# Performance work log

Hardware: AMD Instinct MI355X
Metric: run time of the kernel (lower is better)

The kernel has to match this reference:

```python
import jax, jax.numpy as jnp
import numpy as np

H = 4096
NUM_HEADS = 32
D = 128
SEQ_LEN = 1024
CTX = 4096


def setup_inputs() -> dict:
    key = jax.random.key(0)
    k1, k2, k3, k4 = jax.random.split(key, 4)
    X = jax.random.normal(k1, (SEQ_LEN, H), dtype=jnp.float32)
    # Linear weight [out=3H, in=H]; scale ~1/sqrt(H) so attention logits are O(1)
    W = jax.random.normal(k2, (3 * H, H), dtype=jnp.float32) * (1.0 / np.sqrt(H))
    cache_K = jax.random.normal(k3, (1, CTX, NUM_HEADS, D), dtype=jnp.float32)
    cache_V = jax.random.normal(k4, (1, CTX, NUM_HEADS, D), dtype=jnp.float32)
    return {"X": X, "W": W, "cache_K": cache_K, "cache_V": cache_V}


def reference(X, W, cache_K, cache_V):
    seq_len, h = X.shape
    nh, d = cache_K.shape[2], cache_K.shape[3]
    # fused QKV projection (Linear, no bias): X @ W^T -> [seq_len, 3H]
    qkv = X @ W.T
    q, k, v = jnp.split(qkv, 3, axis=1)
    q = q.reshape(1, seq_len, nh, d)
    k = k.reshape(1, seq_len, nh, d)
    v = v.reshape(1, seq_len, nh, d)
    # concat KV cache along the sequence dim (cache_K[:, :P] with P = full cache)
    k_full = jnp.concatenate([cache_K, k], axis=1)  # [1, ctx+seq, nh, d]
    v_full = jnp.concatenate([cache_V, v], axis=1)
    scale = 1.0 / np.sqrt(d)
    # scores: [1, nh, seq_q, kv_len]
    scores = jnp.einsum("bqhd,bkhd->bhqk", q, k_full) * scale
    weights = jax.nn.softmax(scores, axis=-1)
    out = jnp.einsum("bhqk,bkhd->bqhd", weights, v_full)  # [1, seq, nh, d]
    return out.reshape(seq_len, h)
```

## Files before the change

### kernel.cpp

```cpp
#include <hip/hip_runtime.h>
#include <hip/hip_bf16.h>
#include <stdint.h>

#define H_DIM 4096
#define NH 32
#define HD 128
#define SEQ 1024
#define CTX 4096
#define KVL (CTX + SEQ)
#define W3H (3 * H_DIM)
#define ATTN_SCALE 0.08838834764831845f

typedef short short8 __attribute__((ext_vector_type(8)));
typedef float f32x4 __attribute__((ext_vector_type(4)));

#define GLOAD_LDS16(g, l)                                             \
  __builtin_amdgcn_global_load_lds(                                   \
      (const __attribute__((address_space(1))) void*)(g),             \
      (__attribute__((address_space(3))) void*)(l), 16, 0, 0)

__device__ __forceinline__ unsigned short f2b(float f) {
  union { float f; unsigned u; } v; v.f = f;
  return (unsigned short)((v.u + 0x7FFFu + ((v.u >> 16) & 1u)) >> 16);
}
__device__ __forceinline__ float b2f(unsigned short u) {
  union { unsigned u; float f; } v; v.u = ((unsigned)u) << 16;
  return v.f;
}

__global__ void k_cvt(const float* __restrict__ s, unsigned short* __restrict__ d, int n4) {
  int i = blockIdx.x * blockDim.x + threadIdx.x;
  if (i >= n4) return;
  float4 v = reinterpret_cast<const float4*>(s)[i];
  ushort4 o;
  o.x = f2b(v.x); o.y = f2b(v.y); o.z = f2b(v.z); o.w = f2b(v.w);
  reinterpret_cast<ushort4*>(d)[i] = o;
}

#define BM 128
#define BN 128
#define BK 64
__global__ __launch_bounds__(256, 2) void k_gemm_qkv(
    const unsigned short* __restrict__ A,
    const unsigned short* __restrict__ B,
    unsigned short* __restrict__ C) {
  __shared__ unsigned short As[BM * BK];
  __shared__ unsigned short Bs[BN * BK];
  const int tid = threadIdx.x;
  const int lane = tid & 63;
  const int wid = tid >> 6;
  const int bn = blockIdx.x, bm = blockIdx.y;
  const int wr = wid >> 1, wc = wid & 1;

  f32x4 acc[4][4] = {};

  const int lrow = lane >> 3;
  const int lcol = (lane & 7) * 8;
  const unsigned short* ga = A + (size_t)(bm * BM + wid * 32 + lrow) * H_DIM + lcol;
  const unsigned short* gb = B + (size_t)(bn * BN + wid * 32 + lrow) * H_DIM + lcol;

  for (int kt = 0; kt < H_DIM / BK; ++kt) {
    __syncthreads();
    const unsigned short* gak = ga + kt * BK;
    const unsigned short* gbk = gb + kt * BK;
#pragma unroll
    for (int i = 0; i < 4; ++i) {
      GLOAD_LDS16(gak + i * 8 * H_DIM, As + (wid * 4 + i) * 512);
      GLOAD_LDS16(gbk + i * 8 * H_DIM, Bs + (wid * 4 + i) * 512);
    }
    __syncthreads();
#pragma unroll
    for (int kk = 0; kk < 2; ++kk) {
      short8 af[4], bfr[4];
#pragma unroll
      for (int m = 0; m < 4; ++m)
        af[m] = *reinterpret_cast<const short8*>(
            As + (wr * 64 + m * 16 + (lane & 15)) * BK + kk * 32 + (lane >> 4) * 8);
#pragma unroll
      for (int n = 0; n < 4; ++n)
        bfr[n] = *reinterpret_cast<const short8*>(
            Bs + (wc * 64 + n * 16 + (lane & 15)) * BK + kk * 32 + (lane >> 4) * 8);
#pragma unroll
      for (int m = 0; m < 4; ++m)
#pragma unroll
        for (int n = 0; n < 4; ++n)
          acc[m][n] = __builtin_amdgcn_mfma_f32_16x16x32_bf16(af[m], bfr[n], acc[m][n], 0, 0, 0);
    }
  }
  const int r0 = bm * BM + wr * 64 + (lane >> 4) * 4;
  const int c0 = bn * BN + wc * 64 + (lane & 15);
#pragma unroll
  for (int m = 0; m < 4; ++m)
#pragma unroll
    for (int n = 0; n < 4; ++n)
#pragma unroll
      for (int r = 0; r < 4; ++r)
        C[(size_t)(r0 + m * 16 + r) * W3H + c0 + n * 16] = f2b(acc[m][n][r]);
}

__global__ void k_build_k(const float* __restrict__ cK, const unsigned short* __restrict__ QKV,
                          unsigned short* __restrict__ Kb) {
  int idx = (blockIdx.x * 256 + threadIdx.x) * 4;
  if (idx >= NH * KVL * HD) return;
  int h = idx / (KVL * HD);
  int rem = idx % (KVL * HD);
  int kv = rem / HD;
  int d = rem % HD;
  ushort4 o;
  if (kv < CTX) {
    float4 v = *reinterpret_cast<const float4*>(cK + ((size_t)kv * NH + h) * HD + d);
    o.x = f2b(v.x); o.y = f2b(v.y); o.z = f2b(v.z); o.w = f2b(v.w);
  } else {
    o = *reinterpret_cast<const ushort4*>(QKV + (size_t)(kv - CTX) * W3H + H_DIM + h * HD + d);
  }
  *reinterpret_cast<ushort4*>(Kb + idx) = o;
}

__global__ void k_build_vt(const float* __restrict__ cV, const unsigned short* __restrict__ QKV,
                           unsigned short* __restrict__ Vt) {
  __shared__ unsigned short T[HD][66];
  const int h = blockIdx.y;
  const int kt = blockIdx.x;
  const int t = threadIdx.x;
#pragma unroll
  for (int e = 0; e < 8; ++e) {
    int idx = (t + e * 256) * 4;
    int kvl = idx >> 7;
    int d = idx & 127;
    int kv = kt * 64 + kvl;
    unsigned short a, b, c, w;
    if (kv < CTX) {
      float4 v = *reinterpret_cast<const float4*>(cV + ((size_t)kv * NH + h) * HD + d);
      a = f2b(v.x); b = f2b(v.y); c = f2b(v.z); w = f2b(v.w);
    } else {
      ushort4 u = *reinterpret_cast<const ushort4*>(QKV + (size_t)(kv - CTX) * W3H + 2 * H_DIM + h * HD + d);
      a = u.x; b = u.y; c = u.z; w = u.w;
    }
    T[d][kvl] = a; T[d + 1][kvl] = b; T[d + 2][kvl] = c; T[d + 3][kvl] = w;
  }
  __syncthreads();
#pragma unroll
  for (int e = 0; e < 8; ++e) {
    int idx = (t + e * 256) * 4;
    int d = idx >> 6;
    int kv0 = idx & 63;
    ushort4 o;
    o.x = T[d][kv0]; o.y = T[d][kv0 + 1]; o.z = T[d][kv0 + 2]; o.w = T[d][kv0 + 3];
    *reinterpret_cast<ushort4*>(Vt + ((size_t)h * HD + d) * KVL + kt * 64 + kv0) = o;
  }
}

#define KVT 64
#define NT (KVL / KVT)
#define NT2 (NT / 2)
__global__ __launch_bounds__(256, 2) void k_attn(
    const unsigned short* __restrict__ QKV,
    const unsigned short* __restrict__ Kb,
    const unsigned short* __restrict__ Vt,
    float* __restrict__ A0,
    float* __restrict__ A1,
    float* __restrict__ Mp,
    float* __restrict__ Lp) {
  __shared__ unsigned short Ks[2][KVT * HD];
  __shared__ unsigned short Vs[2][KVT * HD];
  const int tid = threadIdx.x, lane = tid & 63, wid = tid >> 6;
  const int g = lane >> 4;
  const int qi = lane & 15;
  const int id = blockIdx.x;
  const int xcd = id & 7, slot = id >> 3;
  const int h = xcd * 4 + (slot >> 4);
  const int rem = slot & 15;
  const int qt = rem >> 1;
  const int split = rem & 1;
  const int kt0 = split * NT2;
  const int q0 = qt * 128 + wid * 32;

  short8 qf[2][4];
#pragma unroll
  for (int hf = 0; hf < 2; ++hf)
#pragma unroll
    for (int c = 0; c < 4; ++c) {
      short8 q = *reinterpret_cast<const short8*>(
          QKV + (size_t)(q0 + hf * 16 + qi) * W3H + h * HD + c * 32 + g * 8);
      short8 t;
#pragma unroll
      for (int j = 0; j < 8; ++j) t[j] = (short)f2b(b2f((unsigned short)q[j]) * ATTN_SCALE);
      qf[hf][c] = t;
    }

  float m_r[2] = {-1e30f, -1e30f}, l_r[2] = {0.f, 0.f};
  f32x4 acc_o[2][8] = {};

  const char* Kh = (const char*)(Kb + (size_t)h * KVL * HD);
  const char* Vh = (const char*)(Vt + (size_t)h * HD * KVL);

  short8 rK[4], rV[4];

#define LOADR(t)                                                               \
  {                                                                            \
    _Pragma("unroll") for (int i = 0; i < 4; ++i) {                            \
      int c = wid * 4 + i;                                                     \
      int krow = c * 4 + (lane >> 4);                                          \
      int klcb = (16 * (lane & 15)) ^ ((krow & 7) << 4);                       \
      rK[i] = *reinterpret_cast<const short8*>(                                \
          Kh + (size_t)((t) * KVT + krow) * 256 + klcb);                       \
      int vrow = c * 8 + (lane >> 3);                                          \
      int vlcb = (16 * (lane & 7)) ^ ((vrow & 7) << 4);                        \
      rV[i] = *reinterpret_cast<const short8*>(                                \
          Vh + (size_t)vrow * (KVL * 2) + (size_t)(t) * 128 + vlcb);           \
    }                                                                          \
  }
#define WRITE_LDS(b)                                                           \
  {                                                                            \
    _Pragma("unroll") for (int i = 0; i < 4; ++i) {                            \
      *reinterpret_cast<short8*>((char*)Ks[b] + (wid * 4 + i) * 1024 + lane * 16) = rK[i]; \
      *reinterpret_cast<short8*>((char*)Vs[b] + (wid * 4 + i) * 1024 + lane * 16) = rV[i]; \
    }                                                                          \
  }

  LOADR(kt0);
  WRITE_LDS(0);
  __syncthreads();

  const int i0 = ((2 * (g & 1) + 0) * 16 + qi) * 4;
  const int i1 = ((2 * (g & 1) + 1) * 16 + qi) * 4;

  for (int kt = 0; kt < NT2; ++kt) {
    const int cur = kt & 1;
    if (kt + 1 < NT2) LOADR(kt0 + kt + 1);

    f32x4 s[2][4] = {};
#pragma unroll
    for (int n = 0; n < 4; ++n) {
      int row = n * 16 + qi;
#pragma unroll
      for (int c = 0; c < 4; ++c) {
        int cb = (c * 32 + g * 8) * 2;
        short8 kf = *reinterpret_cast<const short8*>(
            (const char*)Ks[cur] + row * 256 + (cb ^ ((row & 7) << 4)));
        s[0][n] = __builtin_amdgcn_mfma_f32_16x16x32_bf16(kf, qf[0][c], s[0][n], 0, 0, 0);
        s[1][n] = __builtin_amdgcn_mfma_f32_16x16x32_bf16(kf, qf[1][c], s[1][n], 0, 0, 0);
      }
    }

    float p[2][4][4];
    int ok = 1;
    float tmax[2];
#pragma unroll
    for (int hf = 0; hf < 2; ++hf) {
      float t0 = s[hf][0][0];
#pragma unroll
      for (int n = 0; n < 4; ++n)
#pragma unroll
        for (int r = 0; r < 4; ++r) t0 = fmaxf(t0, s[hf][n][r]);
      t0 = fmaxf(t0, __shfl_xor(t0, 16, 64));
      t0 = fmaxf(t0, __shfl_xor(t0, 32, 64));
      tmax[hf] = t0;
      ok &= (t0 <= m_r[hf] + 8.0f);
    }
    if (!__all(ok)) {
#pragma unroll
      for (int hf = 0; hf < 2; ++hf) {
        float mn = fmaxf(m_r[hf], tmax[hf]);
        float alpha = __expf(m_r[hf] - mn);
        l_r[hf] *= alpha;
        m_r[hf] = mn;
#pragma unroll
        for (int nd = 0; nd < 8; ++nd) acc_o[hf][nd] *= alpha;
      }
    }
#pragma unroll
    for (int hf = 0; hf < 2; ++hf) {
      float sum = 0.f;
#pragma unroll
      for (int n = 0; n < 4; ++n)
#pragma unroll
        for (int r = 0; r < 4; ++r) {
          p[hf][n][r] = __expf(s[hf][n][r] - m_r[hf]);
          sum += p[hf][n][r];
        }
      sum += __shfl_xor(sum, 16, 64);
      sum += __shfl_xor(sum, 32, 64);
      l_r[hf] += sum;
    }

    unsigned pr[2][4][2];
#pragma unroll
    for (int hf = 0; hf < 2; ++hf)
#pragma unroll
      for (int n = 0; n < 4; ++n)
#pragma unroll
        for (int rr = 0; rr < 2; ++rr) {
          union { __hip_bfloat162 b; unsigned u; } cv;
          cv.b = __float22bfloat162_rn(make_float2(p[hf][n][2 * rr], p[hf][n][2 * rr + 1]));
          pr[hf][n][rr] = cv.u;
        }

#pragma unroll
    for (int kc = 0; kc < 2; ++kc) {
      short8 pv[2];
#pragma unroll
      for (int hf = 0; hf < 2; ++hf) {
        int a0 = __builtin_amdgcn_ds_bpermute(i0, (int)pr[hf][2 * kc][0]);
        int b0 = __builtin_amdgcn_ds_bpermute(i0, (int)pr[hf][2 * kc + 1][0]);
        int a1 = __builtin_amdgcn_ds_bpermute(i0, (int)pr[hf][2 * kc][1]);
        int b1 = __builtin_amdgcn_ds_bpermute(i0, (int)pr[hf][2 * kc + 1][1]);
        int a2 = __builtin_amdgcn_ds_bpermute(i1, (int)pr[hf][2 * kc][0]);
        int b2 = __builtin_amdgcn_ds_bpermute(i1, (int)pr[hf][2 * kc + 1][0]);
        int a3 = __builtin_amdgcn_ds_bpermute(i1, (int)pr[hf][2 * kc][1]);
        int b3 = __builtin_amdgcn_ds_bpermute(i1, (int)pr[hf][2 * kc + 1][1]);
        union { int i[4]; short8 s8; } u;
        u.i[0] = (g < 2) ? a0 : b0;
        u.i[1] = (g < 2) ? a1 : b1;
        u.i[2] = (g < 2) ? a2 : b2;
        u.i[3] = (g < 2) ? a3 : b3;
        pv[hf] = u.s8;
      }

#pragma unroll
      for (int nd = 0; nd < 8; ++nd) {
        int row = nd * 16 + qi;
        int cb = kc * 64 + g * 16;
        short8 vf = *reinterpret_cast<const short8*>(
            (const char*)Vs[cur] + row * 128 + (cb ^ ((row & 7) << 4)));
        acc_o[0][nd] = __builtin_amdgcn_mfma_f32_16x16x32_bf16(vf, pv[0], acc_o[0][nd], 0, 0, 0);
        acc_o[1][nd] = __builtin_amdgcn_mfma_f32_16x16x32_bf16(vf, pv[1], acc_o[1][nd], 0, 0, 0);
      }
    }

    if (kt + 1 < NT2) WRITE_LDS(cur ^ 1);
    __syncthreads();
  }

  float* Op = split ? A1 : A0;
#pragma unroll
  for (int hf = 0; hf < 2; ++hf) {
    float* orow = Op + (size_t)(q0 + hf * 16 + qi) * H_DIM + h * HD;
#pragma unroll
    for (int nd = 0; nd < 8; ++nd)
      *reinterpret_cast<float4*>(orow + nd * 16 + g * 4) =
          *reinterpret_cast<const float4*>(&acc_o[hf][nd]);
    if (g == 0) {
      int q = q0 + hf * 16 + qi;
      Mp[split * (NH * SEQ) + h * SEQ + q] = m_r[hf];
      Lp[split * (NH * SEQ) + h * SEQ + q] = l_r[hf];
    }
  }
#undef LOADR
#undef WRITE_LDS
}

__global__ void k_combine(const float* __restrict__ A1, const float* __restrict__ Mp,
                          const float* __restrict__ Lp, float* __restrict__ out) {
  int i4 = blockIdx.x * 256 + threadIdx.x;
  int q = i4 >> 10;
  int c4 = i4 & 1023;
  int h = c4 >> 5;
  float m0 = Mp[h * SEQ + q], m1 = Mp[NH * SEQ + h * SEQ + q];
  float l0 = Lp[h * SEQ + q], l1 = Lp[NH * SEQ + h * SEQ + q];
  float M = fmaxf(m0, m1);
  float w0 = __expf(m0 - M), w1 = __expf(m1 - M);
  float inv = 1.0f / (w0 * l0 + w1 * l1);
  float4 a0 = reinterpret_cast<const float4*>(out)[i4];
  float4 a1 = reinterpret_cast<const float4*>(A1)[i4];
  float4 o;
  o.x = (w0 * a0.x + w1 * a1.x) * inv;
  o.y = (w0 * a0.y + w1 * a1.y) * inv;
  o.z = (w0 * a0.z + w1 * a1.z) * inv;
  o.w = (w0 * a0.w + w1 * a1.w) * inv;
  reinterpret_cast<float4*>(out)[i4] = o;
}

extern "C" void kernel_launch(void* const* d_in, const int* in_sizes, int n_in,
                              void* d_out, int out_size, void* d_ws, size_t ws_size,
                              hipStream_t stream) {
  const float* X = (const float*)d_in[0];
  const float* W = (const float*)d_in[1];
  const float* cK = (const float*)d_in[2];
  const float* cV = (const float*)d_in[3];
  float* out = (float*)d_out;
  char* ws = (char*)d_ws;

  unsigned short* Xb = (unsigned short*)(ws);
  float* Mp = (float*)(ws);
  float* Lp = (float*)(ws + (256 << 10));
  unsigned short* QKVb = (unsigned short*)(ws + ((size_t)8 << 20));
  unsigned short* Wb = (unsigned short*)(ws + ((size_t)32 << 20));
  unsigned short* Kb = (unsigned short*)(ws + ((size_t)32 << 20));
  unsigned short* Vt = (unsigned short*)(ws + ((size_t)72 << 20));
  float* A1 = (float*)(ws + ((size_t)112 << 20));

  k_cvt<<<(SEQ * H_DIM / 4) / 256, 256, 0, stream>>>(X, Xb, SEQ * H_DIM / 4);
  k_cvt<<<(W3H * H_DIM / 4) / 256, 256, 0, stream>>>(W, Wb, W3H * H_DIM / 4);

  dim3 gg(W3H / BN, SEQ / BM);
  k_gemm_qkv<<<gg, 256, 0, stream>>>(Xb, Wb, QKVb);

  k_build_k<<<(NH * KVL * HD / 4) / 256, 256, 0, stream>>>(cK, QKVb, Kb);
  dim3 gv(KVL / 64, NH);
  k_build_vt<<<gv, 256, 0, stream>>>(cV, QKVb, Vt);

  k_attn<<<SEQ / 128 * NH * 2, 256, 0, stream>>>(QKVb, Kb, Vt, out, A1, Mp, Lp);
  k_combine<<<(SEQ * H_DIM / 4) / 256, 256, 0, stream>>>(A1, Mp, Lp, out);
}
```

Baseline: 351.1 us.

## Software-pipeline attention with async global-to-LDS loads and merge conversion kernels

The attention loop now stages K and V tiles with direct global-to-LDS loads instead of going through registers. Loads are issued two tiles ahead, and the QK^T MFMAs for the next tile are interleaved with the softmax and PV work of the current tile. MFMA sections are wrapped in s_setprio so that matrix work gets issue priority. The two fp32-to-bf16 conversion launches are also merged into one kernel to cut launch overhead. In exchange, register pressure rises from the two live score buffers, and correctness depends on the barriers being placed right relative to the async LDS writes.

```diff
diff --git a/kernel.cpp b/kernel.cpp
--- a/kernel.cpp
+++ b/kernel.cpp
@@ -28,13 +28,20 @@
   return v.f;
 }
 
-__global__ void k_cvt(const float* __restrict__ s, unsigned short* __restrict__ d, int n4) {
-  int i = blockIdx.x * blockDim.x + threadIdx.x;
-  if (i >= n4) return;
-  float4 v = reinterpret_cast<const float4*>(s)[i];
+__global__ void k_cvt2(const float* __restrict__ X, const float* __restrict__ W,
+                       unsigned short* __restrict__ Xb, unsigned short* __restrict__ Wb) {
+  const int nx = SEQ * H_DIM / 4;
+  const int nw = W3H * H_DIM / 4;
+  int i = blockIdx.x * 256 + threadIdx.x;
+  const float* s;
+  unsigned short* d;
+  int j;
+  if (i < nx) { s = X; d = Xb; j = i; }
+  else { j = i - nx; if (j >= nw) return; s = W; d = Wb; }
+  float4 v = reinterpret_cast<const float4*>(s)[j];
   ushort4 o;
   o.x = f2b(v.x); o.y = f2b(v.y); o.z = f2b(v.z); o.w = f2b(v.w);
-  reinterpret_cast<ushort4*>(d)[i] = o;
+  reinterpret_cast<ushort4*>(d)[j] = o;
 }
 
 #define BM 128
@@ -194,142 +201,146 @@
   const char* Kh = (const char*)(Kb + (size_t)h * KVL * HD);
   const char* Vh = (const char*)(Vt + (size_t)h * HD * KVL);
 
-  short8 rK[4], rV[4];
-
-#define LOADR(t)                                                               \
+#define STAGE_K(t, b)                                                          \
   {                                                                            \
     _Pragma("unroll") for (int i = 0; i < 4; ++i) {                            \
       int c = wid * 4 + i;                                                     \
       int krow = c * 4 + (lane >> 4);                                          \
       int klcb = (16 * (lane & 15)) ^ ((krow & 7) << 4);                       \
-      rK[i] = *reinterpret_cast<const short8*>(                                \
-          Kh + (size_t)((t) * KVT + krow) * 256 + klcb);                       \
+      GLOAD_LDS16(Kh + (size_t)((t) * KVT + krow) * 256 + klcb,                \
+                  (char*)Ks[b] + c * 1024);                                    \
+    }                                                                          \
+  }
+#define STAGE_V(t, b)                                                          \
+  {                                                                            \
+    _Pragma("unroll") for (int i = 0; i < 4; ++i) {                            \
+      int c = wid * 4 + i;                                                     \
       int vrow = c * 8 + (lane >> 3);                                          \
       int vlcb = (16 * (lane & 7)) ^ ((vrow & 7) << 4);                        \
-      rV[i] = *reinterpret_cast<const short8*>(                                \
-          Vh + (size_t)vrow * (KVL * 2) + (size_t)(t) * 128 + vlcb);           \
-    }                                                                          \
-  }
-#define WRITE_LDS(b)                                                           \
+      GLOAD_LDS16(Vh + (size_t)vrow * (KVL * 2) + (size_t)(t) * 128 + vlcb,    \
+                  (char*)Vs[b] + c * 1024);                                    \
+    }                                                                          \
+  }
+#define QKT(buf, S)                                                            \
   {                                                                            \
-    _Pragma("unroll") for (int i = 0; i < 4; ++i) {                            \
-      *reinterpret_cast<short8*>((char*)Ks[b] + (wid * 4 + i) * 1024 + lane * 16) = rK[i]; \
-      *reinterpret_cast<short8*>((char*)Vs[b] + (wid * 4 + i) * 1024 + lane * 16) = rV[i]; \
-    }                                                                          \
-  }
-
-  LOADR(kt0);
-  WRITE_LDS(0);
-  __syncthreads();
+    _Pragma("unroll") for (int n = 0; n < 4; ++n) {                            \
+      S[0][n] = (f32x4){0.f, 0.f, 0.f, 0.f};                                   \
+      S[1][n] = (f32x4){0.f, 0.f, 0.f, 0.f};                                   \
+    }                                                                          \
+    __builtin_amdgcn_s_setprio(1);                                             \
+    _Pragma("unroll") for (int n = 0; n < 4; ++n) {                            \
+      int row = n * 16 + qi;                                                   \
+      _Pragma("unroll") for (int c = 0; c < 4; ++c) {                          \
+        int cb = (c * 32 + g * 8) * 2;                                         \
+        short8 kf = *reinterpret_cast<const short8*>(                          \
+            (const char*)Ks[buf] + row * 256 + (cb ^ ((row & 7) << 4)));       \
+        S[0][n] = __builtin_amdgcn_mfma_f32_16x16x32_bf16(kf, qf[0][c], S[0][n], 0, 0, 0); \
+        S[1][n] = __builtin_amdgcn_mfma_f32_16x16x32_bf16(kf, qf[1][c], S[1][n], 0, 0, 0); \
+      }                                                                        \
+    }                                                                          \
+    __builtin_amdgcn_s_setprio(0);                                             \
+  }
 
   const int i0 = ((2 * (g & 1) + 0) * 16 + qi) * 4;
   const int i1 = ((2 * (g & 1) + 1) * 16 + qi) * 4;
 
-  for (int kt = 0; kt < NT2; ++kt) {
-    const int cur = kt & 1;
-    if (kt + 1 < NT2) LOADR(kt0 + kt + 1);
-
-    f32x4 s[2][4] = {};
-#pragma unroll
-    for (int n = 0; n < 4; ++n) {
-      int row = n * 16 + qi;
-#pragma unroll
-      for (int c = 0; c < 4; ++c) {
-        int cb = (c * 32 + g * 8) * 2;
-        short8 kf = *reinterpret_cast<const short8*>(
-            (const char*)Ks[cur] + row * 256 + (cb ^ ((row & 7) << 4)));
-        s[0][n] = __builtin_amdgcn_mfma_f32_16x16x32_bf16(kf, qf[0][c], s[0][n], 0, 0, 0);
-        s[1][n] = __builtin_amdgcn_mfma_f32_16x16x32_bf16(kf, qf[1][c], s[1][n], 0, 0, 0);
-      }
-    }
-
-    float p[2][4][4];
-    int ok = 1;
-    float tmax[2];
-#pragma unroll
-    for (int hf = 0; hf < 2; ++hf) {
-      float t0 = s[hf][0][0];
-#pragma unroll
-      for (int n = 0; n < 4; ++n)
-#pragma unroll
-        for (int r = 0; r < 4; ++r) t0 = fmaxf(t0, s[hf][n][r]);
-      t0 = fmaxf(t0, __shfl_xor(t0, 16, 64));
-      t0 = fmaxf(t0, __shfl_xor(t0, 32, 64));
-      tmax[hf] = t0;
-      ok &= (t0 <= m_r[hf] + 8.0f);
-    }
-    if (!__all(ok)) {
-#pragma unroll
-      for (int hf = 0; hf < 2; ++hf) {
-        float mn = fmaxf(m_r[hf], tmax[hf]);
-        float alpha = __expf(m_r[hf] - mn);
-        l_r[hf] *= alpha;
-        m_r[hf] = mn;
-#pragma unroll
-        for (int nd = 0; nd < 8; ++nd) acc_o[hf][nd] *= alpha;
-      }
-    }
-#pragma unroll
-    for (int hf = 0; hf < 2; ++hf) {
-      float sum = 0.f;
-#pragma unroll
-      for (int n = 0; n < 4; ++n)
-#pragma unroll
-        for (int r = 0; r < 4; ++r) {
-          p[hf][n][r] = __expf(s[hf][n][r] - m_r[hf]);
-          sum += p[hf][n][r];
-        }
-      sum += __shfl_xor(sum, 16, 64);
-      sum += __shfl_xor(sum, 32, 64);
-      l_r[hf] += sum;
-    }
-
-    unsigned pr[2][4][2];
-#pragma unroll
-    for (int hf = 0; hf < 2; ++hf)
-#pragma unroll
-      for (int n = 0; n < 4; ++n)
-#pragma unroll
-        for (int rr = 0; rr < 2; ++rr) {
-          union { __hip_bfloat162 b; unsigned u; } cv;
-          cv.b = __float22bfloat162_rn(make_float2(p[hf][n][2 * rr], p[hf][n][2 * rr + 1]));
-          pr[hf][n][rr] = cv.u;
-        }
-
-#pragma unroll
-    for (int kc = 0; kc < 2; ++kc) {
-      short8 pv[2];
-#pragma unroll
-      for (int hf = 0; hf < 2; ++hf) {
-        int a0 = __builtin_amdgcn_ds_bpermute(i0, (int)pr[hf][2 * kc][0]);
-        int b0 = __builtin_amdgcn_ds_bpermute(i0, (int)pr[hf][2 * kc + 1][0]);
-        int a1 = __builtin_amdgcn_ds_bpermute(i0, (int)pr[hf][2 * kc][1]);
-        int b1 = __builtin_amdgcn_ds_bpermute(i0, (int)pr[hf][2 * kc + 1][1]);
-        int a2 = __builtin_amdgcn_ds_bpermute(i1, (int)pr[hf][2 * kc][0]);
-        int b2 = __builtin_amdgcn_ds_bpermute(i1, (int)pr[hf][2 * kc + 1][0]);
-        int a3 = __builtin_amdgcn_ds_bpermute(i1, (int)pr[hf][2 * kc][1]);
-        int b3 = __builtin_amdgcn_ds_bpermute(i1, (int)pr[hf][2 * kc + 1][1]);
-        union { int i[4]; short8 s8; } u;
-        u.i[0] = (g < 2) ? a0 : b0;
-        u.i[1] = (g < 2) ? a1 : b1;
-        u.i[2] = (g < 2) ? a2 : b2;
-        u.i[3] = (g < 2) ? a3 : b3;
-        pv[hf] = u.s8;
-      }
-
-#pragma unroll
-      for (int nd = 0; nd < 8; ++nd) {
-        int row = nd * 16 + qi;
-        int cb = kc * 64 + g * 16;
-        short8 vf = *reinterpret_cast<const short8*>(
-            (const char*)Vs[cur] + row * 128 + (cb ^ ((row & 7) << 4)));
-        acc_o[0][nd] = __builtin_amdgcn_mfma_f32_16x16x32_bf16(vf, pv[0], acc_o[0][nd], 0, 0, 0);
-        acc_o[1][nd] = __builtin_amdgcn_mfma_f32_16x16x32_bf16(vf, pv[1], acc_o[1][nd], 0, 0, 0);
-      }
-    }
-
-    if (kt + 1 < NT2) WRITE_LDS(cur ^ 1);
-    __syncthreads();
+#define SMPV(S, vb)                                                            \
+  {                                                                            \
+    float p[2][4][4];                                                          \
+    int okv = 1;                                                               \
+    float tmax[2];                                                             \
+    _Pragma("unroll") for (int hf = 0; hf < 2; ++hf) {                         \
+      float t0 = S[hf][0][0];                                                  \
+      _Pragma("unroll") for (int n = 0; n < 4; ++n)                            \
+        _Pragma("unroll") for (int r = 0; r < 4; ++r)                          \
+          t0 = fmaxf(t0, S[hf][n][r]);                                         \
+      t0 = fmaxf(t0, __shfl_xor(t0, 16, 64));                                  \
+      t0 = fmaxf(t0, __shfl_xor(t0, 32, 64));                                  \
+      tmax[hf] = t0;                                                           \
+      okv &= (t0 <= m_r[hf] + 8.0f);                                           \
+    }                                                                          \
+    if (!__all(okv)) {                                                         \
+      _Pragma("unroll") for (int hf = 0; hf < 2; ++hf) {                       \
+        float mn = fmaxf(m_r[hf], tmax[hf]);                                   \
+        float alpha = __expf(m_r[hf] - mn);                                    \
+        l_r[hf] *= alpha;                                                      \
+        m_r[hf] = mn;                                                          \
+        _Pragma("unroll") for (int nd = 0; nd < 8; ++nd) acc_o[hf][nd] *= alpha; \
+      }                                                                        \
+    }                                                                          \
+    _Pragma("unroll") for (int hf = 0; hf < 2; ++hf) {                         \
+      float sum = 0.f;                                                         \
+      _Pragma("unroll") for (int n = 0; n < 4; ++n)                            \
+        _Pragma("unroll") for (int r = 0; r < 4; ++r) {                        \
+          p[hf][n][r] = __expf(S[hf][n][r] - m_r[hf]);                         \
+          sum += p[hf][n][r];                                                  \
+        }                                                                      \
+      sum += __shfl_xor(sum, 16, 64);                                          \
+      sum += __shfl_xor(sum, 32, 64);                                          \
+      l_r[hf] += sum;                                                          \
+    }                                                                          \
+    unsigned pr[2][4][2];                                                      \
+    _Pragma("unroll") for (int hf = 0; hf < 2; ++hf)                           \
+      _Pragma("unroll") for (int n = 0; n < 4; ++n)                            \
+        _Pragma("unroll") for (int rr = 0; rr < 2; ++rr) {                     \
+          union { __hip_bfloat162 b; unsigned u; } cv;                         \
+          cv.b = __float22bfloat162_rn(                                        \
+              make_float2(p[hf][n][2 * rr], p[hf][n][2 * rr + 1]));            \
+          pr[hf][n][rr] = cv.u;                                                \
+        }                                                                      \
+    _Pragma("unroll") for (int kc = 0; kc < 2; ++kc) {                         \
+      short8 pv[2];                                                            \
+      _Pragma("unroll") for (int hf = 0; hf < 2; ++hf) {                       \
+        int a0 = __builtin_amdgcn_ds_bpermute(i0, (int)pr[hf][2 * kc][0]);     \
+        int b0 = __builtin_amdgcn_ds_bpermute(i0, (int)pr[hf][2 * kc + 1][0]); \
+        int a1 = __builtin_amdgcn_ds_bpermute(i0, (int)pr[hf][2 * kc][1]);     \
+        int b1 = __builtin_amdgcn_ds_bpermute(i0, (int)pr[hf][2 * kc + 1][1]); \
+        int a2 = __builtin_amdgcn_ds_bpermute(i1, (int)pr[hf][2 * kc][0]);     \
+        int b2 = __builtin_amdgcn_ds_bpermute(i1, (int)pr[hf][2 * kc + 1][0]); \
+        int a3 = __builtin_amdgcn_ds_bpermute(i1, (int)pr[hf][2 * kc][1]);     \
+        int b3 = __builtin_amdgcn_ds_bpermute(i1, (int)pr[hf][2 * kc + 1][1]); \
+        union { int i[4]; short8 s8; } u;                                      \
+        u.i[0] = (g < 2) ? a0 : b0;                                            \
+        u.i[1] = (g < 2) ? a1 : b1;                                            \
+        u.i[2] = (g < 2) ? a2 : b2;                                            \
+        u.i[3] = (g < 2) ? a3 : b3;                                            \
+        pv[hf] = u.s8;                                                         \
+      }                                                                        \
+      __builtin_amdgcn_s_setprio(1);                                           \
+      _Pragma("unroll") for (int nd = 0; nd < 8; ++nd) {                       \
+        int row = nd * 16 + qi;                                                \
+        int cb = kc * 64 + g * 16;                                             \
+        short8 vf = *reinterpret_cast<const short8*>(                          \
+            (const char*)Vs[vb] + row * 128 + (cb ^ ((row & 7) << 4)));        \
+        acc_o[0][nd] = __builtin_amdgcn_mfma_f32_16x16x32_bf16(vf, pv[0], acc_o[0][nd], 0, 0, 0); \
+        acc_o[1][nd] = __builtin_amdgcn_mfma_f32_16x16x32_bf16(vf, pv[1], acc_o[1][nd], 0, 0, 0); \
+      }                                                                        \
+      __builtin_amdgcn_s_setprio(0);                                           \
+    }                                                                          \
+  }
+
+#define BODY(t, SC, SN)                                                        \
+  {                                                                            \
+    const int cur = (t) & 1;                                                   \
+    if ((t) + 2 < NT2) STAGE_K(kt0 + (t) + 2, cur);                            \
+    if ((t) + 1 < NT2) QKT(cur ^ 1, SN);                                       \
+    SMPV(SC, cur);                                                             \
+    __syncthreads();                                                           \
+    if ((t) + 2 < NT2) STAGE_V(kt0 + (t) + 2, cur);                            \
+  }
+
+  STAGE_K(kt0, 0);
+  STAGE_V(kt0, 0);
+  STAGE_K(kt0 + 1, 1);
+  STAGE_V(kt0 + 1, 1);
+  __syncthreads();
+
+  f32x4 sA[2][4], sB[2][4];
+  QKT(0, sA);
+
+  for (int tt = 0; tt < NT2; tt += 2) {
+    BODY(tt, sA, sB);
+    BODY(tt + 1, sB, sA);
   }
 
   float* Op = split ? A1 : A0;
@@ -346,8 +357,11 @@
       Lp[split * (NH * SEQ) + h * SEQ + q] = l_r[hf];
     }
   }
-#undef LOADR
-#undef WRITE_LDS
+#undef STAGE_K
+#undef STAGE_V
+#undef QKT
+#undef SMPV
+#undef BODY
 }
 
 __global__ void k_combine(const float* __restrict__ A1, const float* __restrict__ Mp,
@@ -390,8 +404,8 @@
   unsigned short* Vt = (unsigned short*)(ws + ((size_t)72 << 20));
   float* A1 = (float*)(ws + ((size_t)112 << 20));
 
-  k_cvt<<<(SEQ * H_DIM / 4) / 256, 256, 0, stream>>>(X, Xb, SEQ * H_DIM / 4);
-  k_cvt<<<(W3H * H_DIM / 4) / 256, 256, 0, stream>>>(W, Wb, W3H * H_DIM / 4);
+  int ncvt = (SEQ * H_DIM + W3H * H_DIM) / 4;
+  k_cvt2<<<(ncvt + 255) / 256, 256, 0, stream>>>(X, W, Xb, Wb);
 
   dim3 gg(W3H / BN, SEQ / BM);
   k_gemm_qkv<<<gg, 256, 0, stream>>>(Xb, Wb, QKVb);
```

Result: no change. 354.4 us (+0.9%).
